# Kernel tuning notes

Measured on AMD Instinct MI355X. Metric: run time of the kernel, lower is better.

The kernel has to match this reference:

```python
import jax, jax.numpy as jnp
import numpy as np

# config constants
B, L, ENC_IN = 8, 512, 7
D_MODEL = 768
EXPAND = 2
D_INNER = D_MODEL * EXPAND          # 1536
DT_RANK = (D_MODEL + 15) // 16      # 48
N_STATE = 16                         # configs.d_ff acts as SSM state size
K_CONV = 4
E_LAYERS = 2
C_OUT = 7
PRED_LEN = 96
EPS = 1e-5


def rmsnorm(x, w):
    return x * jax.lax.rsqrt(jnp.mean(x * x, axis=-1, keepdims=True) + EPS) * w


def silu(x):
    return x * jax.nn.sigmoid(x)


def positional_embedding(l, d):
    pos = np.arange(l, dtype=np.float32)[:, None]
    div = np.exp(np.arange(0, d, 2, dtype=np.float32) * (-np.log(10000.0) / d))
    pe = np.zeros((l, d), dtype=np.float32)
    pe[:, 0::2] = np.sin(pos * div)
    pe[:, 1::2] = np.cos(pos * div)
    return jnp.asarray(pe)


def causal_dwconv(x, w, b):
    # x: [b, d, l], w: [d, 1, k]; torch pads k-1 both sides then slices [:l] == left-pad k-1
    y = jax.lax.conv_general_dilated(
        x, w, window_strides=(1,), padding=[(K_CONV - 1, 0)],
        dimension_numbers=('NCH', 'OIH', 'NCH'), feature_group_count=D_INNER)
    return y + b[None, :, None]


def selective_scan(u, delta, A, Bm, Cm, Dp):
    # u, delta: [b,l,d]; A: [d,n]; Bm, Cm: [b,l,n]; Dp: [d]
    deltaA = jnp.exp(jnp.einsum('bld,dn->bldn', delta, A))          # [b,l,d,n]
    deltaBu = (delta * u)[..., None] * Bm[:, :, None, :]             # [b,l,d,n]

    def step(xc, inp):
        dA, dBu, Ct = inp                                            # [b,d,n],[b,d,n],[b,n]
        xc = dA * xc + dBu
        return xc, jnp.einsum('bdn,bn->bd', xc, Ct)

    b, l, d = u.shape
    x0 = jnp.zeros((b, d, A.shape[1]), u.dtype)
    _, ys = jax.lax.scan(step, x0, (jnp.moveaxis(deltaA, 1, 0),
                                    jnp.moveaxis(deltaBu, 1, 0),
                                    jnp.moveaxis(Cm, 1, 0)))
    y = jnp.moveaxis(ys, 0, 1)                                       # [b,l,d]
    return y + u * Dp


def mamba_block(x, in_w, conv_w, conv_b, xproj_w, dtproj_w, dtproj_b, A_log, Dp, outproj_w):
    xr = x @ in_w.T                                                  # [b,l,2*d_inner]
    xs, res = xr[..., :D_INNER], xr[..., D_INNER:]
    xs = causal_dwconv(jnp.swapaxes(xs, 1, 2), conv_w, conv_b)
    xs = silu(jnp.swapaxes(xs, 1, 2))
    # ssm
    A = -jnp.exp(A_log)
    x_dbl = xs @ xproj_w.T                                           # [b,l,dt_rank+2n]
    delta = x_dbl[..., :DT_RANK]
    Bm = x_dbl[..., DT_RANK:DT_RANK + N_STATE]
    Cm = x_dbl[..., DT_RANK + N_STATE:]
    delta = jax.nn.softplus(delta @ dtproj_w.T + dtproj_b)
    y = selective_scan(xs, delta, A, Bm, Cm, Dp)
    y = y * silu(res)
    return y @ outproj_w.T


def setup_inputs() -> dict:
    key = jax.random.key(0)
    ks = iter(jax.random.split(key, 32))
    s = 0.02
    d = {}
    d['x'] = jax.random.normal(next(ks), (B, L, ENC_IN), jnp.float32)
    d['token_w'] = jax.random.normal(next(ks), (D_MODEL, ENC_IN, 3), jnp.float32) * s
    d['time_w'] = jax.random.normal(next(ks), (D_MODEL, 1), jnp.float32) * s
    d['norm_w'] = jnp.ones((E_LAYERS, D_MODEL), jnp.float32)
    d['in_w'] = jax.random.normal(next(ks), (E_LAYERS, 2 * D_INNER, D_MODEL), jnp.float32) * s
    d['conv_w'] = jax.random.normal(next(ks), (E_LAYERS, D_INNER, 1, K_CONV), jnp.float32) * s
    d['conv_b'] = jnp.zeros((E_LAYERS, D_INNER), jnp.float32)
    d['xproj_w'] = jax.random.normal(next(ks), (E_LAYERS, DT_RANK + 2 * N_STATE, D_INNER), jnp.float32) * s
    d['dtproj_w'] = jax.random.normal(next(ks), (E_LAYERS, D_INNER, DT_RANK), jnp.float32) * s
    d['dtproj_b'] = jnp.zeros((E_LAYERS, D_INNER), jnp.float32)
    A = np.tile(np.arange(1, N_STATE + 1, dtype=np.float32)[None, :], (D_INNER, 1))
    d['A_log'] = jnp.tile(jnp.log(jnp.asarray(A))[None], (E_LAYERS, 1, 1))
    d['Dp'] = jnp.ones((E_LAYERS, D_INNER), jnp.float32)
    d['outproj_w'] = jax.random.normal(next(ks), (E_LAYERS, D_MODEL, D_INNER), jnp.float32) * s
    d['final_norm_w'] = jnp.ones((D_MODEL,), jnp.float32)
    d['out_w'] = jax.random.normal(next(ks), (C_OUT, D_MODEL), jnp.float32) * s
    return d


def reference(x, token_w, time_w, norm_w, in_w, conv_w, conv_b, xproj_w,
              dtproj_w, dtproj_b, A_log, Dp, outproj_w, final_norm_w, out_w):
    # instance normalization (mean/std detached)
    mean_enc = jax.lax.stop_gradient(jnp.mean(x, axis=1, keepdims=True))
    xc = x - mean_enc
    std_enc = jax.lax.stop_gradient(jnp.sqrt(jnp.var(xc, axis=1, keepdims=True) + 1e-5))
    xc = xc / std_enc
    # DataEmbedding: circular conv token emb + sinusoidal pos + timeF linear
    xp = jnp.pad(jnp.swapaxes(xc, 1, 2), ((0, 0), (0, 0), (1, 1)), mode='wrap')
    tok = jax.lax.conv_general_dilated(xp, token_w, (1,), 'VALID',
                                       dimension_numbers=('NCH', 'OIH', 'NCH'))
    tok = jnp.swapaxes(tok, 1, 2)                                    # [b,l,d_model]
    x_mark = (jnp.arange(L, dtype=x.dtype) / L)[None, :, None]       # [1,l,1]
    h = tok + positional_embedding(L, D_MODEL)[None] + x_mark @ time_w.T
    for e in range(E_LAYERS):
        h = mamba_block(rmsnorm(h, norm_w[e]), in_w[e], conv_w[e], conv_b[e],
                        xproj_w[e], dtproj_w[e], dtproj_b[e], A_log[e], Dp[e],
                        outproj_w[e]) + h
    h = rmsnorm(h, final_norm_w)
    out = h @ out_w.T
    out = out * std_enc + mean_enc
    return out[:, -PRED_LEN:, :]
```

## Files before the change

kernel.cpp:

```cpp
#include <hip/hip_runtime.h>
#include <hip/hip_bf16.h>
#include <math.h>

#define BSZ 8
#define LSEQ 512
#define ENC_IN 7
#define D_MODEL 768
#define D_INNER 1536
#define DT_RANK 48
#define N_STATE 16
#define K_CONV 4
#define E_LAYERS 2
#define C_OUT 7
#define PRED_LEN 96
#define EPSV 1e-5f
#define XN 80
#define KSPLIT 4

#define ROWS (BSZ*LSEQ)
#define NC 16
#define CL (LSEQ/NC)
#define NTILE (LSEQ/16)
#define LOG2E 1.44269504088896f

typedef __bf16 bf16x8 __attribute__((ext_vector_type(8)));
typedef float  f32x4  __attribute__((ext_vector_type(4)));

__device__ __forceinline__ float fexp2(float x) {
    float r;
    asm("v_exp_f32 %0, %1" : "=v"(r) : "v"(x));
    return r;
}

__device__ __forceinline__ float block_sum(float v, float* tmp) {
    #pragma unroll
    for (int off = 32; off > 0; off >>= 1) v += __shfl_down(v, off);
    int lane = threadIdx.x & 63, wid = threadIdx.x >> 6;
    __syncthreads();
    if (lane == 0) tmp[wid] = v;
    __syncthreads();
    return tmp[0] + tmp[1] + tmp[2] + tmp[3];
}

__global__ __launch_bounds__(256) void cvt_all(const float* __restrict__ in_w,
                                               const float* __restrict__ outw,
                                               const float* __restrict__ xpw,
                                               const float* __restrict__ dtw,
                                               __hip_bfloat16* __restrict__ inw_bf,
                                               __hip_bfloat16* __restrict__ outw_bf,
                                               __hip_bfloat16* __restrict__ xpw_bf,
                                               __hip_bfloat16* __restrict__ dtw_bf) {
    const int N1 = E_LAYERS*2*D_INNER*D_MODEL;
    const int N2 = E_LAYERS*D_MODEL*D_INNER;
    const int N3 = E_LAYERS*XN*D_INNER;
    const int N4 = E_LAYERS*D_INNER*64;
    int i = blockIdx.x*256 + threadIdx.x;
    if (i < N1) {
        inw_bf[i] = __float2bfloat16(in_w[i]);
    } else if (i < N1+N2) {
        int j = i - N1; outw_bf[j] = __float2bfloat16(outw[j]);
    } else if (i < N1+N2+N3) {
        int j = i - N1 - N2; xpw_bf[j] = __float2bfloat16(xpw[j]);
    } else if (i < N1+N2+N3+N4) {
        int j = i - N1 - N2 - N3;
        int r = j >> 6, c = j & 63;
        dtw_bf[j] = __float2bfloat16(c < DT_RANK ? dtw[r*DT_RANK + c] : 0.f);
    }
}

__global__ __launch_bounds__(256) void stats_kernel(const float* __restrict__ x,
                                                    float* __restrict__ mean,
                                                    float* __restrict__ stdv) {
    int bc = blockIdx.x;
    int b = bc / ENC_IN, c = bc % ENC_IN;
    __shared__ float tmp[4];
    float s = 0.f, sq = 0.f;
    for (int l = threadIdx.x; l < LSEQ; l += 256) {
        float v = x[((size_t)(b*LSEQ + l))*ENC_IN + c];
        s += v; sq += v*v;
    }
    s = block_sum(s, tmp);
    sq = block_sum(sq, tmp);
    if (threadIdx.x == 0) {
        float m = s / LSEQ;
        float var = sq / LSEQ - m*m;
        if (var < 0.f) var = 0.f;
        mean[bc] = m;
        stdv[bc] = sqrtf(var + EPSV);
    }
}

__global__ __launch_bounds__(256) void embed_kernel(const float* __restrict__ x,
                                                    const float* __restrict__ token_w,
                                                    const float* __restrict__ time_w,
                                                    const float* __restrict__ mean,
                                                    const float* __restrict__ stdv,
                                                    float* __restrict__ h) {
    int bl = blockIdx.x;
    int b = bl >> 9, l = bl & 511;
    __shared__ float sxc[ENC_IN*3];
    if (threadIdx.x < ENC_IN*3) {
        int c = threadIdx.x / 3, k = threadIdx.x % 3;
        int lk = (l + k - 1) & 511;
        float v = x[((size_t)(b*LSEQ + lk))*ENC_IN + c];
        sxc[threadIdx.x] = (v - mean[b*ENC_IN + c]) / stdv[b*ENC_IN + c];
    }
    __syncthreads();
    #pragma unroll
    for (int i = 0; i < 3; i++) {
        int d = threadIdx.x + i*256;
        float acc = 0.f;
        const float* w = token_w + (size_t)d*21;
        #pragma unroll
        for (int t = 0; t < 21; t++) acc += sxc[t] * w[t];
        int d2 = d & ~1;
        float div = __expf((float)d2 * (-9.210340371976184f / (float)D_MODEL));
        float ang = (float)l * div;
        float pe = (d & 1) ? cosf(ang) : sinf(ang);
        float tm = ((float)l / (float)LSEQ) * time_w[d];
        h[(size_t)bl*D_MODEL + d] = acc + pe + tm;
    }
}

__global__ __launch_bounds__(256) void rmsnorm_bf16(const float* __restrict__ h,
                                                    const float* __restrict__ w,
                                                    __hip_bfloat16* __restrict__ xn) {
    size_t base = (size_t)blockIdx.x * D_MODEL;
    __shared__ float tmp[4];
    float ss = 0.f;
    for (int k = threadIdx.x; k < D_MODEL; k += 256) { float v = h[base+k]; ss += v*v; }
    ss = block_sum(ss, tmp);
    float inv = rsqrtf(ss / (float)D_MODEL + EPSV);
    for (int k = threadIdx.x; k < D_MODEL; k += 256)
        xn[base+k] = __float2bfloat16(h[base+k]*inv*w[k]);
}

template<int FUSE>
__global__ __launch_bounds__(256) void gemm_mfma(const __hip_bfloat16* __restrict__ A,
                                                 const __hip_bfloat16* __restrict__ Bw,
                                                 float* __restrict__ C,
                                                 int K,
                                                 const float* __restrict__ bias,
                                                 float* __restrict__ C2,
                                                 __hip_bfloat16* __restrict__ Cb) {
    __shared__ __align__(16) __hip_bfloat16 As[128*32];
    __shared__ __align__(16) __hip_bfloat16 Bs[128*32];
    int tid = threadIdx.x, lane = tid & 63, w = tid >> 6;
    int gx = gridDim.x;
    int nwg = gx * gridDim.y;
    int orig = blockIdx.y*gx + blockIdx.x;
    int swz = (orig & 7)*(nwg >> 3) + (orig >> 3);
    int m0 = (swz / gx) * 128, n0 = (swz % gx) * 128;
    int wr = w >> 1, wc = w & 1;
    int kq = lane >> 4, rr = lane & 15;

    f32x4 acc[4][4];
    #pragma unroll
    for (int i = 0; i < 4; i++)
        #pragma unroll
        for (int j = 0; j < 4; j++) acc[i][j] = (f32x4){0.f,0.f,0.f,0.f};

    const char* Ab = (const char*)A;
    const char* Bb = (const char*)Bw;
    char* AsB = (char*)As;
    char* BsB = (char*)Bs;

    int c0 = tid, c1 = tid + 256;
    int r0 = c0 >> 2, q0 = (c0 & 3) ^ ((r0 >> 1) & 3);
    int r1 = c1 >> 2, q1 = (c1 & 3) ^ ((r1 >> 1) & 3);
    int sw = (kq ^ ((rr >> 1) & 3)) * 16;

    for (int k0 = 0; k0 < K; k0 += 32) {
        __builtin_amdgcn_global_load_lds(
            (const __attribute__((address_space(1))) unsigned int*)(Ab + ((size_t)(m0+r0)*K + k0 + q0*8)*2),
            (__attribute__((address_space(3))) unsigned int*)(AsB + c0*16), 16, 0, 0);
        __builtin_amdgcn_global_load_lds(
            (const __attribute__((address_space(1))) unsigned int*)(Ab + ((size_t)(m0+r1)*K + k0 + q1*8)*2),
            (__attribute__((address_space(3))) unsigned int*)(AsB + c1*16), 16, 0, 0);
        __builtin_amdgcn_global_load_lds(
            (const __attribute__((address_space(1))) unsigned int*)(Bb + ((size_t)(n0+r0)*K + k0 + q0*8)*2),
            (__attribute__((address_space(3))) unsigned int*)(BsB + c0*16), 16, 0, 0);
        __builtin_amdgcn_global_load_lds(
            (const __attribute__((address_space(1))) unsigned int*)(Bb + ((size_t)(n0+r1)*K + k0 + q1*8)*2),
            (__attribute__((address_space(3))) unsigned int*)(BsB + c1*16), 16, 0, 0);
        __syncthreads();

        bf16x8 af[4], bfr[4];
        #pragma unroll
        for (int mi = 0; mi < 4; mi++) af[mi]  = *(const bf16x8*)(AsB + (wr*64 + mi*16 + rr)*64 + sw);
        #pragma unroll
        for (int ni = 0; ni < 4; ni++) bfr[ni] = *(const bf16x8*)(BsB + (wc*64 + ni*16 + rr)*64 + sw);
        #pragma unroll
        for (int mi = 0; mi < 4; mi++)
            #pragma unroll
            for (int ni = 0; ni < 4; ni++)
                acc[mi][ni] = __builtin_amdgcn_mfma_f32_16x16x32_bf16(af[mi], bfr[ni], acc[mi][ni], 0, 0, 0);
        __syncthreads();
    }

    #pragma unroll
    for (int mi = 0; mi < 4; mi++) {
        #pragma unroll
        for (int ni = 0; ni < 4; ni++) {
            int row0 = m0 + wr*64 + mi*16;
            int col  = n0 + wc*64 + ni*16 + rr;
            if (FUSE == 1) {
                float4 v4;
                #pragma unroll
                for (int r = 0; r < 4; r++) {
                    float v = acc[mi][ni][r] + bias[col];
                    ((float*)&v4)[r] = fmaxf(v, 0.f) + log1pf(__expf(-fabsf(v)));
                }
                *(float4*)&C[((size_t)(row0 >> 4)*D_INNER + col)*16 + kq*4] = v4;
            } else if (FUSE == 3) {
                if (col >= D_INNER) {
                    float4 v4;
                    #pragma unroll
                    for (int r = 0; r < 4; r++) {
                        float v = acc[mi][ni][r];
                        ((float*)&v4)[r] = v / (1.f + __expf(-v));
                    }
                    *(float4*)&C2[((size_t)(row0 >> 4)*D_INNER + (col - D_INNER))*16 + kq*4] = v4;
                } else {
                    #pragma unroll
                    for (int r = 0; r < 4; r++) {
                        int row = row0 + kq*4 + r;
                        Cb[(size_t)row*D_INNER + col] = __float2bfloat16(acc[mi][ni][r]);
                    }
                }
            }
        }
    }
}

__global__ __launch_bounds__(256) void gemm_outproj(const __hip_bfloat16* __restrict__ A,
                                                    const __hip_bfloat16* __restrict__ Bw,
                                                    float* __restrict__ C) {
    __shared__ __align__(16) __hip_bfloat16 As[128*32];
    __shared__ __align__(16) __hip_bfloat16 Bs[64*32];
    int tid = threadIdx.x, lane = tid & 63, w = tid >> 6;
    int gx = gridDim.x;
    int nwg = gx * gridDim.y;
    int orig = blockIdx.y*gx + blockIdx.x;
    int swz = (orig & 7)*(nwg >> 3) + (orig >> 3);
    int m0 = (swz / gx) * 128, n0 = (swz % gx) * 64;
    int wr = w >> 1, wc = w & 1;
    int kq = lane >> 4, rr = lane & 15;
    const int K = D_INNER;

    f32x4 acc[4][2];
    #pragma unroll
    for (int i = 0; i < 4; i++)
        #pragma unroll
        for (int j = 0; j < 2; j++) acc[i][j] = (f32x4){0.f,0.f,0.f,0.f};

    const char* Ab = (const char*)A;
    const char* Bb = (const char*)Bw;
    char* AsB = (char*)As;
    char* BsB = (char*)Bs;

    int cA0 = tid, cA1 = tid + 256;
    int rA0 = cA0 >> 2, qA0 = (cA0 & 3) ^ ((rA0 >> 1) & 3);
    int rA1 = cA1 >> 2, qA1 = (cA1 & 3) ^ ((rA1 >> 1) & 3);
    int rB = tid >> 2,  qB  = (tid & 3) ^ ((rB >> 1) & 3);
    int sw = (kq ^ ((rr >> 1) & 3)) * 16;

    for (int k0 = 0; k0 < K; k0 += 32) {
        __builtin_amdgcn_global_load_lds(
            (const __attribute__((address_space(1))) unsigned int*)(Ab + ((size_t)(m0+rA0)*K + k0 + qA0*8)*2),
            (__attribute__((address_space(3))) unsigned int*)(AsB + cA0*16), 16, 0, 0);
        __builtin_amdgcn_global_load_lds(
            (const __attribute__((address_space(1))) unsigned int*)(Ab + ((size_t)(m0+rA1)*K + k0 + qA1*8)*2),
            (__attribute__((address_space(3))) unsigned int*)(AsB + cA1*16), 16, 0, 0);
        __builtin_amdgcn_global_load_lds(
            (const __attribute__((address_space(1))) unsigned int*)(Bb + ((size_t)(n0+rB)*K + k0 + qB*8)*2),
            (__attribute__((address_space(3))) unsigned int*)(BsB + tid*16), 16, 0, 0);
        __syncthreads();

        bf16x8 af[4], bfr[2];
        #pragma unroll
        for (int mi = 0; mi < 4; mi++) af[mi]  = *(const bf16x8*)(AsB + (wr*64 + mi*16 + rr)*64 + sw);
        #pragma unroll
        for (int ni = 0; ni < 2; ni++) bfr[ni] = *(const bf16x8*)(BsB + (wc*32 + ni*16 + rr)*64 + sw);
        #pragma unroll
        for (int mi = 0; mi < 4; mi++)
            #pragma unroll
            for (int ni = 0; ni < 2; ni++)
                acc[mi][ni] = __builtin_amdgcn_mfma_f32_16x16x32_bf16(af[mi], bfr[ni], acc[mi][ni], 0, 0, 0);
        __syncthreads();
    }

    #pragma unroll
    for (int mi = 0; mi < 4; mi++) {
        #pragma unroll
        for (int ni = 0; ni < 2; ni++) {
            #pragma unroll
            for (int r = 0; r < 4; r++) {
                int row = m0 + wr*64 + mi*16 + kq*4 + r;
                int col = n0 + wc*32 + ni*16 + rr;
                size_t o = (size_t)row*D_MODEL + col;
                C[o] = acc[mi][ni][r] + C[o];
            }
        }
    }
}

__global__ __launch_bounds__(256) void gemm_xproj(const __hip_bfloat16* __restrict__ A,
                                                  const __hip_bfloat16* __restrict__ W,
                                                  float* __restrict__ P) {
    __shared__ __align__(16) __hip_bfloat16 As[64*64];
    __shared__ __align__(16) __hip_bfloat16 Bs[96*64];
    int tid = threadIdx.x, lane = tid & 63, w = tid >> 6;
    int m0 = blockIdx.x * 64;
    int k0 = blockIdx.y * (D_INNER / KSPLIT);
    int kq = lane >> 4, rr = lane & 15;
    f32x4 acc[5];
    #pragma unroll
    for (int i = 0; i < 5; i++) acc[i] = (f32x4){0.f,0.f,0.f,0.f};
    const char* Ab = (const char*)A;
    const char* Wb = (const char*)W;
    char* AsB = (char*)As;
    char* BsB = (char*)Bs;

    for (int kk = k0; kk < k0 + D_INNER/KSPLIT; kk += 64) {
        #pragma unroll
        for (int cA = 0; cA < 2; cA++) {
            int idx = cA*256 + tid;
            int r = idx >> 3, q = (idx & 7) ^ (r & 7);
            __builtin_amdgcn_global_load_lds(
                (const __attribute__((address_space(1))) unsigned int*)(Ab + ((size_t)(m0+r)*D_INNER + kk + q*8)*2),
                (__attribute__((address_space(3))) unsigned int*)(AsB + idx*16), 16, 0, 0);
        }
        #pragma unroll
        for (int cB = 0; cB < 3; cB++) {
            int idx = cB*256 + tid;
            int r = idx >> 3, q = (idx & 7) ^ (r & 7);
            int rs = r < XN ? r : XN-1;
            __builtin_amdgcn_global_load_lds(
                (const __attribute__((address_space(1))) unsigned int*)(Wb + ((size_t)rs*D_INNER + kk + q*8)*2),
                (__attribute__((address_space(3))) unsigned int*)(BsB + idx*16), 16, 0, 0);
        }
        __syncthreads();
        #pragma unroll
        for (int kh = 0; kh < 2; kh++) {
            bf16x8 a = *(const bf16x8*)(AsB + (w*16 + rr)*128 + (((kh*4 + kq) ^ (rr & 7)))*16);
            #pragma unroll
            for (int ni = 0; ni < 5; ni++) {
                bf16x8 b = *(const bf16x8*)(BsB + (ni*16 + rr)*128 + (((kh*4 + kq) ^ (rr & 7)))*16);
                acc[ni] = __builtin_amdgcn_mfma_f32_16x16x32_bf16(a, b, acc[ni], 0, 0, 0);
            }
        }
        __syncthreads();
    }
    float* Cp = P + (size_t)blockIdx.y * ROWS * XN;
    #pragma unroll
    for (int ni = 0; ni < 5; ni++)
        #pragma unroll
        for (int r = 0; r < 4; r++) {
            int row = m0 + w*16 + kq*4 + r;
            int col = ni*16 + rr;
            Cp[(size_t)row*XN + col] = acc[ni][r];
        }
}

__global__ __launch_bounds__(256) void xproj_reduce(const float* __restrict__ P,
                                                    float* __restrict__ xdbl,
                                                    __hip_bfloat16* __restrict__ xdbl_bf) {
    int idx = blockIdx.x*256 + threadIdx.x;
    int col = idx % 96, row = idx / 96;
    if (row >= ROWS) return;
    const size_t RX = (size_t)ROWS*XN;
    if (col < XN) {
        size_t o = (size_t)row*XN + col;
        float s = P[o] + P[RX + o] + P[2*RX + o] + P[3*RX + o];
        xdbl[o] = s;
        if (col < DT_RANK) xdbl_bf[(size_t)row*64 + col] = __float2bfloat16(s);
    } else {
        xdbl_bf[(size_t)row*64 + col - 32] = __float2bfloat16(0.f);
    }
}

__global__ __launch_bounds__(256) void dwconv_silu(const __hip_bfloat16* __restrict__ xs,
                                                   const float* __restrict__ cw,
                                                   const float* __restrict__ cb,
                                                   __hip_bfloat16* __restrict__ u_bf) {
    int idx = blockIdx.x*256 + threadIdx.x;
    int dg = idx % (D_INNER/8);
    int t  = idx / (D_INNER/8);
    if (t >= ROWS) return;
    int d0 = dg*8;
    int l = t & 511, b = t >> 9;
    bf16x8 rows[K_CONV];
    #pragma unroll
    for (int k = 0; k < K_CONV; k++) {
        int ll = l - (K_CONV-1) + k;
        if (ll >= 0) rows[k] = *(const bf16x8*)(xs + ((size_t)(b*LSEQ + ll))*D_INNER + d0);
        else { bf16x8 z = {}; rows[k] = z; }
    }
    bf16x8 outv;
    #pragma unroll
    for (int j = 0; j < 8; j++) {
        int d = d0 + j;
        const float4 w4 = *(const float4*)(cw + d*K_CONV);
        float acc = cb[d]
                  + (float)rows[0][j]*w4.x + (float)rows[1][j]*w4.y
                  + (float)rows[2][j]*w4.z + (float)rows[3][j]*w4.w;
        float v = acc / (1.f + __expf(-acc));
        outv[j] = (__bf16)v;
    }
    *(bf16x8*)(u_bf + (size_t)t*D_INNER + d0) = outv;
}

__global__ __launch_bounds__(256) void scan_p1(const __hip_bfloat16* __restrict__ u,
                                               const float* __restrict__ delta_blk,
                                               const float* __restrict__ xdbl,
                                               const float* __restrict__ A_log,
                                               float* __restrict__ xfin,
                                               float* __restrict__ sumdlt) {
    int d = blockIdx.x*256 + threadIdx.x;
    int c = blockIdx.y, b = blockIdx.z;
    int l0 = c*CL;
    float A2[N_STATE], xs[N_STATE];
    const float* al = A_log + d*N_STATE;
    #pragma unroll
    for (int n = 0; n < N_STATE; n++) {
        A2[n] = -__expf(al[n]) * LOG2E;
        xs[n] = 0.f;
    }
    const __hip_bfloat16* pu = u + (size_t)(b*LSEQ + l0)*D_INNER + d;
    const float* pB = xdbl + (size_t)(b*LSEQ + l0)*XN + DT_RANK;
    float sd = 0.f;
    #pragma unroll
    for (int tt = 0; tt < 2; tt++) {
        const float* db = delta_blk + ((size_t)(b*NTILE + (l0>>4) + tt)*D_INNER + d)*16;
        float dl[16];
        #pragma unroll
        for (int q = 0; q < 4; q++) {
            f32x4 v = *(const f32x4*)(db + q*4);
            dl[q*4+0]=v[0]; dl[q*4+1]=v[1]; dl[q*4+2]=v[2]; dl[q*4+3]=v[3];
        }
        #pragma unroll
        for (int i = 0; i < 16; i++) {
            float dlt = dl[i];
            float uu = __bfloat162float(*pu); pu += D_INNER;
            float du = dlt*uu;
            sd += dlt;
            #pragma unroll
            for (int n = 0; n < N_STATE; n++)
                xs[n] = fexp2(dlt*A2[n])*xs[n] + du*pB[n];
            pB += XN;
        }
    }
    float* px = xfin + (size_t)((b*NC + c)*N_STATE)*D_INNER + d;
    #pragma unroll
    for (int n = 0; n < N_STATE; n++) px[n*D_INNER] = xs[n];
    sumdlt[(size_t)(b*NC + c)*D_INNER + d] = sd;
}

__global__ __launch_bounds__(256) void scan_p2(float* __restrict__ xfin,
                                               const float* __restrict__ sumdlt,
                                               const float* __restrict__ A_log) {
    int idx = blockIdx.x*256 + threadIdx.x;
    int d = idx % D_INNER;
    int r = idx / D_INNER;
    int n = r & 15;
    int b = r >> 4;
    float A2 = -__expf(A_log[d*N_STATE + n]) * LOG2E;
    float cr = 0.f;
    for (int c = 1; c < NC; c++) {
        size_t jp = (size_t)(b*NC + c - 1);
        float xf = xfin[(jp*N_STATE + n)*D_INNER + d];
        float s  = sumdlt[jp*D_INNER + d];
        cr = fexp2(A2 * s) * cr + xf;
        xfin[(jp*N_STATE + n)*D_INNER + d] = cr;
    }
}

__global__ __launch_bounds__(256) void scan_p3(const __hip_bfloat16* __restrict__ u,
                                               const float* __restrict__ delta_blk,
                                               const float* __restrict__ gres_blk,
                                               const float* __restrict__ xdbl,
                                               const float* __restrict__ A_log,
                                               const float* __restrict__ Dp,
                                               const float* __restrict__ carry,
                                               __hip_bfloat16* __restrict__ ygate) {
    int d = blockIdx.x*256 + threadIdx.x;
    int c = blockIdx.y, b = blockIdx.z;
    int l0 = c*CL;
    float A2[N_STATE], xs[N_STATE];
    const float* al = A_log + d*N_STATE;
    #pragma unroll
    for (int n = 0; n < N_STATE; n++) A2[n] = -__expf(al[n]) * LOG2E;
    if (c == 0) {
        #pragma unroll
        for (int n = 0; n < N_STATE; n++) xs[n] = 0.f;
    } else {
        const float* pc = carry + (size_t)((b*NC + c - 1)*N_STATE)*D_INNER + d;
        #pragma unroll
        for (int n = 0; n < N_STATE; n++) xs[n] = pc[n*D_INNER];
    }
    float Dv = Dp[d];
    const __hip_bfloat16* pu = u + (size_t)(b*LSEQ + l0)*D_INNER + d;
    const float* pB = xdbl + (size_t)(b*LSEQ + l0)*XN + DT_RANK;
    __hip_bfloat16* py = ygate + (size_t)(b*LSEQ + l0)*D_INNER + d;
    #pragma unroll
    for (int tt = 0; tt < 2; tt++) {
        size_t tb = (size_t)(b*NTILE + (l0>>4) + tt)*D_INNER + d;
        const float* db = delta_blk + tb*16;
        const float* gb = gres_blk  + tb*16;
        float dl[16], gr[16];
        #pragma unroll
        for (int q = 0; q < 4; q++) {
            f32x4 v = *(const f32x4*)(db + q*4);
            dl[q*4+0]=v[0]; dl[q*4+1]=v[1]; dl[q*4+2]=v[2]; dl[q*4+3]=v[3];
            f32x4 g = *(const f32x4*)(gb + q*4);
            gr[q*4+0]=g[0]; gr[q*4+1]=g[1]; gr[q*4+2]=g[2]; gr[q*4+3]=g[3];
        }
        #pragma unroll
        for (int i = 0; i < 16; i++) {
            float dlt = dl[i];
            float uu = __bfloat162float(*pu); pu += D_INNER;
            float du = dlt*uu;
            float acc = 0.f;
            #pragma unroll
            for (int n = 0; n < N_STATE; n++) {
                xs[n] = fexp2(dlt*A2[n])*xs[n] + du*pB[n];
                acc += xs[n]*pB[N_STATE + n];
            }
            pB += XN;
            float y = acc + uu*Dv;
            *py = __float2bfloat16(y * gr[i]); py += D_INNER;
        }
    }
}

__global__ __launch_bounds__(256) void final_kernel(const float* __restrict__ h,
                                                    const float* __restrict__ fnw,
                                                    const float* __restrict__ out_w,
                                                    const float* __restrict__ mean,
                                                    const float* __restrict__ stdv,
                                                    float* __restrict__ out) {
    int bid = blockIdx.x;
    int b = bid / PRED_LEN, lo = bid % PRED_LEN;
    int l = LSEQ - PRED_LEN + lo;
    const float* row = h + ((size_t)(b*LSEQ + l))*D_MODEL;
    __shared__ float tmp[4];
    float ss = 0.f;
    for (int k = threadIdx.x; k < D_MODEL; k += 256) { float v = row[k]; ss += v*v; }
    ss = block_sum(ss, tmp);
    float inv = rsqrtf(ss / (float)D_MODEL + EPSV);
    float acc[C_OUT] = {};
    for (int k = threadIdx.x; k < D_MODEL; k += 256) {
        float hn = row[k]*fnw[k];
        #pragma unroll
        for (int c = 0; c < C_OUT; c++) acc[c] += hn*out_w[c*D_MODEL + k];
    }
    #pragma unroll
    for (int c = 0; c < C_OUT; c++) {
        float s = block_sum(acc[c], tmp);
        if (threadIdx.x == 0)
            out[((size_t)(b*PRED_LEN + lo))*C_OUT + c] = s*inv*stdv[b*ENC_IN + c] + mean[b*ENC_IN + c];
    }
}

extern "C" void kernel_launch(void* const* d_in, const int* in_sizes, int n_in,
                              void* d_out, int out_size, void* d_ws, size_t ws_size,
                              hipStream_t stream) {
    const float* x        = (const float*)d_in[0];
    const float* token_w  = (const float*)d_in[1];
    const float* time_w   = (const float*)d_in[2];
    const float* norm_w   = (const float*)d_in[3];
    const float* in_w     = (const float*)d_in[4];
    const float* conv_w   = (const float*)d_in[5];
    const float* conv_b   = (const float*)d_in[6];
    const float* xproj_w  = (const float*)d_in[7];
    const float* dtproj_w = (const float*)d_in[8];
    const float* dtproj_b = (const float*)d_in[9];
    const float* A_log    = (const float*)d_in[10];
    const float* Dp       = (const float*)d_in[11];
    const float* outproj_w= (const float*)d_in[12];
    const float* final_nw = (const float*)d_in[13];
    const float* out_w    = (const float*)d_in[14];
    float* out = (float*)d_out;

    float* ws   = (float*)d_ws;
    float* mean = ws;
    float* stdv = ws + 64;
    float* h    = ws + 128;
    float* gres = h    + (size_t)ROWS*D_MODEL;
    float* delta= gres + (size_t)ROWS*D_INNER;
    float* xdbl = delta+ (size_t)ROWS*D_INNER;
    float* sumd = xdbl + (size_t)ROWS*XN;
    float* xfin = sumd + (size_t)BSZ*NC*D_INNER;
    float* pout = xfin + (size_t)BSZ*NC*D_INNER*N_STATE;
    float* fend = pout + (size_t)KSPLIT*ROWS*XN;
    __hip_bfloat16* xn_bf  = (__hip_bfloat16*)fend;
    __hip_bfloat16* xs_bf  = xn_bf + (size_t)ROWS*D_MODEL;
    __hip_bfloat16* u_bf   = xs_bf + (size_t)ROWS*D_INNER;
    __hip_bfloat16* ygate  = u_bf  + (size_t)ROWS*D_INNER;
    __hip_bfloat16* xdbl_bf= ygate + (size_t)ROWS*D_INNER;
    __hip_bfloat16* inw_bf = xdbl_bf+ (size_t)ROWS*64;
    __hip_bfloat16* outw_bf= inw_bf + (size_t)E_LAYERS*2*D_INNER*D_MODEL;
    __hip_bfloat16* xpw_bf = outw_bf+ (size_t)E_LAYERS*D_MODEL*D_INNER;
    __hip_bfloat16* dtw_bf = xpw_bf + (size_t)E_LAYERS*XN*D_INNER;

    {
        const int NT = E_LAYERS*2*D_INNER*D_MODEL + E_LAYERS*D_MODEL*D_INNER
                     + E_LAYERS*XN*D_INNER + E_LAYERS*D_INNER*64;
        cvt_all<<<(NT+255)/256, 256, 0, stream>>>(in_w, outproj_w, xproj_w, dtproj_w,
                                                  inw_bf, outw_bf, xpw_bf, dtw_bf);
    }

    stats_kernel<<<BSZ*ENC_IN, 256, 0, stream>>>(x, mean, stdv);
    embed_kernel<<<ROWS, 256, 0, stream>>>(x, token_w, time_w, mean, stdv, h);

    for (int e = 0; e < E_LAYERS; e++) {
        rmsnorm_bf16<<<ROWS, 256, 0, stream>>>(h, norm_w + e*D_MODEL, xn_bf);
        gemm_mfma<3><<<dim3(2*D_INNER/128, ROWS/128), 256, 0, stream>>>(
            xn_bf, inw_bf + (size_t)e*2*D_INNER*D_MODEL, nullptr, D_MODEL,
            nullptr, gres, xs_bf);
        dwconv_silu<<<(ROWS*(D_INNER/8) + 255)/256, 256, 0, stream>>>(
            xs_bf, conv_w + (size_t)e*D_INNER*K_CONV, conv_b + e*D_INNER, u_bf);
        gemm_xproj<<<dim3(ROWS/64, KSPLIT), 256, 0, stream>>>(
            u_bf, xpw_bf + (size_t)e*XN*D_INNER, pout);
        xproj_reduce<<<(ROWS*96 + 255)/256, 256, 0, stream>>>(pout, xdbl, xdbl_bf);
        gemm_mfma<1><<<dim3(D_INNER/128, ROWS/128), 256, 0, stream>>>(
            xdbl_bf, dtw_bf + (size_t)e*D_INNER*64, delta, 64,
            dtproj_b + e*D_INNER, nullptr, nullptr);
        const float* Alog_e = A_log + (size_t)e*D_INNER*N_STATE;
        scan_p1<<<dim3(D_INNER/256, NC, BSZ), 256, 0, stream>>>(
            u_bf, delta, xdbl, Alog_e, xfin, sumd);
        scan_p2<<<(BSZ*D_INNER*N_STATE)/256, 256, 0, stream>>>(
            xfin, sumd, Alog_e);
        scan_p3<<<dim3(D_INNER/256, NC, BSZ), 256, 0, stream>>>(
            u_bf, delta, gres, xdbl, Alog_e, Dp + (size_t)e*D_INNER, xfin, ygate);
        gemm_outproj<<<dim3(D_MODEL/64, ROWS/128), 256, 0, stream>>>(
            ygate, outw_bf + (size_t)e*D_MODEL*D_INNER, h);
    }

    final_kernel<<<BSZ*PRED_LEN, 256, 0, stream>>>(h, final_nw, out_w, mean, stdv, out);
}
```

Baseline: 400.2 us.

## Fuse dt projection and softplus into scan kernels, widen in-proj K tile

The dt_proj GEMM and its delta buffer are removed. Each scan thread now holds its 48 dt weights in registers and computes delta = softplus(bias + x_dbl·w) inline in both scan passes, so delta is computed twice but never written to or read from memory. The gate buffer is stored as bf16 instead of fp32, and the in-projection GEMM uses a 64-wide K tile with a new swizzle. The cost is extra FMAs and register pressure in the scan kernels (48 extra registers plus per-step dot products), which may reduce occupancy.

New measurement: 471.7 us. 17.9% more time.

```diff
diff --git a/kernel.cpp b/kernel.cpp
--- a/kernel.cpp
+++ b/kernel.cpp
@@ -31,6 +31,9 @@
     asm("v_exp_f32 %0, %1" : "=v"(r) : "v"(x));
     return r;
 }
+__device__ __forceinline__ float softplusf(float v) {
+    return fmaxf(v, 0.f) + log1pf(__expf(-fabsf(v)));
+}
 
 __device__ __forceinline__ float block_sum(float v, float* tmp) {
     #pragma unroll
@@ -45,15 +48,12 @@
 __global__ __launch_bounds__(256) void cvt_all(const float* __restrict__ in_w,
                                                const float* __restrict__ outw,
                                                const float* __restrict__ xpw,
-                                               const float* __restrict__ dtw,
                                                __hip_bfloat16* __restrict__ inw_bf,
                                                __hip_bfloat16* __restrict__ outw_bf,
-                                               __hip_bfloat16* __restrict__ xpw_bf,
-                                               __hip_bfloat16* __restrict__ dtw_bf) {
+                                               __hip_bfloat16* __restrict__ xpw_bf) {
     const int N1 = E_LAYERS*2*D_INNER*D_MODEL;
     const int N2 = E_LAYERS*D_MODEL*D_INNER;
     const int N3 = E_LAYERS*XN*D_INNER;
-    const int N4 = E_LAYERS*D_INNER*64;
     int i = blockIdx.x*256 + threadIdx.x;
     if (i < N1) {
         inw_bf[i] = __float2bfloat16(in_w[i]);
@@ -61,10 +61,6 @@
         int j = i - N1; outw_bf[j] = __float2bfloat16(outw[j]);
     } else if (i < N1+N2+N3) {
         int j = i - N1 - N2; xpw_bf[j] = __float2bfloat16(xpw[j]);
-    } else if (i < N1+N2+N3+N4) {
-        int j = i - N1 - N2 - N3;
-        int r = j >> 6, c = j & 63;
-        dtw_bf[j] = __float2bfloat16(c < DT_RANK ? dtw[r*DT_RANK + c] : 0.f);
     }
 }
 
@@ -135,16 +131,13 @@
         xn[base+k] = __float2bfloat16(h[base+k]*inv*w[k]);
 }
 
-template<int FUSE>
-__global__ __launch_bounds__(256) void gemm_mfma(const __hip_bfloat16* __restrict__ A,
-                                                 const __hip_bfloat16* __restrict__ Bw,
-                                                 float* __restrict__ C,
-                                                 int K,
-                                                 const float* __restrict__ bias,
-                                                 float* __restrict__ C2,
-                                                 __hip_bfloat16* __restrict__ Cb) {
-    __shared__ __align__(16) __hip_bfloat16 As[128*32];
-    __shared__ __align__(16) __hip_bfloat16 Bs[128*32];
+__global__ __launch_bounds__(256) void gemm_inproj(const __hip_bfloat16* __restrict__ A,
+                                                   const __hip_bfloat16* __restrict__ Bw,
+                                                   __hip_bfloat16* __restrict__ Cxs,
+                                                   __hip_bfloat16* __restrict__ Cg) {
+    __shared__ __align__(16) __hip_bfloat16 As[128*64];
+    __shared__ __align__(16) __hip_bfloat16 Bs[128*64];
+    const int K = D_MODEL;
     int tid = threadIdx.x, lane = tid & 63, w = tid >> 6;
     int gx = gridDim.x;
     int nwg = gx * gridDim.y;
@@ -165,36 +158,35 @@
     char* AsB = (char*)As;
     char* BsB = (char*)Bs;
 
-    int c0 = tid, c1 = tid + 256;
-    int r0 = c0 >> 2, q0 = (c0 & 3) ^ ((r0 >> 1) & 3);
-    int r1 = c1 >> 2, q1 = (c1 & 3) ^ ((r1 >> 1) & 3);
-    int sw = (kq ^ ((rr >> 1) & 3)) * 16;
-
-    for (int k0 = 0; k0 < K; k0 += 32) {
-        __builtin_amdgcn_global_load_lds(
-            (const __attribute__((address_space(1))) unsigned int*)(Ab + ((size_t)(m0+r0)*K + k0 + q0*8)*2),
-            (__attribute__((address_space(3))) unsigned int*)(AsB + c0*16), 16, 0, 0);
-        __builtin_amdgcn_global_load_lds(
-            (const __attribute__((address_space(1))) unsigned int*)(Ab + ((size_t)(m0+r1)*K + k0 + q1*8)*2),
-            (__attribute__((address_space(3))) unsigned int*)(AsB + c1*16), 16, 0, 0);
-        __builtin_amdgcn_global_load_lds(
-            (const __attribute__((address_space(1))) unsigned int*)(Bb + ((size_t)(n0+r0)*K + k0 + q0*8)*2),
-            (__attribute__((address_space(3))) unsigned int*)(BsB + c0*16), 16, 0, 0);
-        __builtin_amdgcn_global_load_lds(
-            (const __attribute__((address_space(1))) unsigned int*)(Bb + ((size_t)(n0+r1)*K + k0 + q1*8)*2),
-            (__attribute__((address_space(3))) unsigned int*)(BsB + c1*16), 16, 0, 0);
+    for (int k0 = 0; k0 < K; k0 += 64) {
+        #pragma unroll
+        for (int c = 0; c < 4; c++) {
+            int idx = c*256 + tid;
+            int r = idx >> 3, q = idx & 7;
+            int qs = q ^ (r & 7);
+            __builtin_amdgcn_global_load_lds(
+                (const __attribute__((address_space(1))) unsigned int*)(Ab + ((size_t)(m0+r)*K + k0 + qs*8)*2),
+                (__attribute__((address_space(3))) unsigned int*)(AsB + idx*16), 16, 0, 0);
+            __builtin_amdgcn_global_load_lds(
+                (const __attribute__((address_space(1))) unsigned int*)(Bb + ((size_t)(n0+r)*K + k0 + qs*8)*2),
+                (__attribute__((address_space(3))) unsigned int*)(BsB + idx*16), 16, 0, 0);
+        }
         __syncthreads();
 
-        bf16x8 af[4], bfr[4];
-        #pragma unroll
-        for (int mi = 0; mi < 4; mi++) af[mi]  = *(const bf16x8*)(AsB + (wr*64 + mi*16 + rr)*64 + sw);
-        #pragma unroll
-        for (int ni = 0; ni < 4; ni++) bfr[ni] = *(const bf16x8*)(BsB + (wc*64 + ni*16 + rr)*64 + sw);
-        #pragma unroll
-        for (int mi = 0; mi < 4; mi++)
-            #pragma unroll
-            for (int ni = 0; ni < 4; ni++)
-                acc[mi][ni] = __builtin_amdgcn_mfma_f32_16x16x32_bf16(af[mi], bfr[ni], acc[mi][ni], 0, 0, 0);
+        #pragma unroll
+        for (int kh = 0; kh < 2; kh++) {
+            int ch = ((kh*4 + kq) ^ (rr & 7)) * 16;
+            bf16x8 af[4], bfr[4];
+            #pragma unroll
+            for (int mi = 0; mi < 4; mi++) af[mi]  = *(const bf16x8*)(AsB + (wr*64 + mi*16 + rr)*128 + ch);
+            #pragma unroll
+            for (int ni = 0; ni < 4; ni++) bfr[ni] = *(const bf16x8*)(BsB + (wc*64 + ni*16 + rr)*128 + ch);
+            #pragma unroll
+            for (int mi = 0; mi < 4; mi++)
+                #pragma unroll
+                for (int ni = 0; ni < 4; ni++)
+                    acc[mi][ni] = __builtin_amdgcn_mfma_f32_16x16x32_bf16(af[mi], bfr[ni], acc[mi][ni], 0, 0, 0);
+        }
         __syncthreads();
     }
 
@@ -204,29 +196,20 @@
         for (int ni = 0; ni < 4; ni++) {
             int row0 = m0 + wr*64 + mi*16;
             int col  = n0 + wc*64 + ni*16 + rr;
-            if (FUSE == 1) {
-                float4 v4;
+            if (col >= D_INNER) {
+                __hip_bfloat16 g4[4];
                 #pragma unroll
                 for (int r = 0; r < 4; r++) {
-                    float v = acc[mi][ni][r] + bias[col];
-                    ((float*)&v4)[r] = fmaxf(v, 0.f) + log1pf(__expf(-fabsf(v)));
+                    float v = acc[mi][ni][r];
+                    g4[r] = __float2bfloat16(v / (1.f + __expf(-v)));
                 }
-                *(float4*)&C[((size_t)(row0 >> 4)*D_INNER + col)*16 + kq*4] = v4;
-            } else if (FUSE == 3) {
-                if (col >= D_INNER) {
-                    float4 v4;
-                    #pragma unroll
-                    for (int r = 0; r < 4; r++) {
-                        float v = acc[mi][ni][r];
-                        ((float*)&v4)[r] = v / (1.f + __expf(-v));
-                    }
-                    *(float4*)&C2[((size_t)(row0 >> 4)*D_INNER + (col - D_INNER))*16 + kq*4] = v4;
-                } else {
-                    #pragma unroll
-                    for (int r = 0; r < 4; r++) {
-                        int row = row0 + kq*4 + r;
-                        Cb[(size_t)row*D_INNER + col] = __float2bfloat16(acc[mi][ni][r]);
-                    }
+                int cd = col - D_INNER;
+                *(uint2*)&Cg[((size_t)(row0 >> 4)*D_INNER + cd)*16 + kq*4] = *(uint2*)g4;
+            } else {
+                #pragma unroll
+                for (int r = 0; r < 4; r++) {
+                    int row = row0 + kq*4 + r;
+                    Cxs[(size_t)row*D_INNER + col] = __float2bfloat16(acc[mi][ni][r]);
                 }
             }
         }
@@ -364,20 +347,11 @@
 }
 
 __global__ __launch_bounds__(256) void xproj_reduce(const float* __restrict__ P,
-                                                    float* __restrict__ xdbl,
-                                                    __hip_bfloat16* __restrict__ xdbl_bf) {
+                                                    float* __restrict__ xdbl) {
     int idx = blockIdx.x*256 + threadIdx.x;
-    int col = idx % 96, row = idx / 96;
-    if (row >= ROWS) return;
+    if (idx >= ROWS*XN) return;
     const size_t RX = (size_t)ROWS*XN;
-    if (col < XN) {
-        size_t o = (size_t)row*XN + col;
-        float s = P[o] + P[RX + o] + P[2*RX + o] + P[3*RX + o];
-        xdbl[o] = s;
-        if (col < DT_RANK) xdbl_bf[(size_t)row*64 + col] = __float2bfloat16(s);
-    } else {
-        xdbl_bf[(size_t)row*64 + col - 32] = __float2bfloat16(0.f);
-    }
+    xdbl[idx] = P[idx] + P[RX + idx] + P[2*RX + idx] + P[3*RX + idx];
 }
 
 __global__ __launch_bounds__(256) void dwconv_silu(const __hip_bfloat16* __restrict__ xs,
@@ -412,44 +386,41 @@
 }
 
 __global__ __launch_bounds__(256) void scan_p1(const __hip_bfloat16* __restrict__ u,
-                                               const float* __restrict__ delta_blk,
                                                const float* __restrict__ xdbl,
+                                               const float* __restrict__ dtw,
+                                               const float* __restrict__ dtb,
                                                const float* __restrict__ A_log,
                                                float* __restrict__ xfin,
                                                float* __restrict__ sumdlt) {
     int d = blockIdx.x*256 + threadIdx.x;
     int c = blockIdx.y, b = blockIdx.z;
     int l0 = c*CL;
-    float A2[N_STATE], xs[N_STATE];
+    float A2[N_STATE], xs[N_STATE], wd[DT_RANK];
     const float* al = A_log + d*N_STATE;
     #pragma unroll
     for (int n = 0; n < N_STATE; n++) {
         A2[n] = -__expf(al[n]) * LOG2E;
         xs[n] = 0.f;
     }
+    const float* pw = dtw + (size_t)d*DT_RANK;
+    #pragma unroll
+    for (int k = 0; k < DT_RANK; k++) wd[k] = pw[k];
+    float bias = dtb[d];
     const __hip_bfloat16* pu = u + (size_t)(b*LSEQ + l0)*D_INNER + d;
-    const float* pB = xdbl + (size_t)(b*LSEQ + l0)*XN + DT_RANK;
+    const float* pX = xdbl + (size_t)(b*LSEQ + l0)*XN;
     float sd = 0.f;
-    #pragma unroll
-    for (int tt = 0; tt < 2; tt++) {
-        const float* db = delta_blk + ((size_t)(b*NTILE + (l0>>4) + tt)*D_INNER + d)*16;
-        float dl[16];
-        #pragma unroll
-        for (int q = 0; q < 4; q++) {
-            f32x4 v = *(const f32x4*)(db + q*4);
-            dl[q*4+0]=v[0]; dl[q*4+1]=v[1]; dl[q*4+2]=v[2]; dl[q*4+3]=v[3];
-        }
-        #pragma unroll
-        for (int i = 0; i < 16; i++) {
-            float dlt = dl[i];
-            float uu = __bfloat162float(*pu); pu += D_INNER;
-            float du = dlt*uu;
-            sd += dlt;
-            #pragma unroll
-            for (int n = 0; n < N_STATE; n++)
-                xs[n] = fexp2(dlt*A2[n])*xs[n] + du*pB[n];
-            pB += XN;
-        }
+    for (int i = 0; i < CL; i++) {
+        float v = bias;
+        #pragma unroll
+        for (int k = 0; k < DT_RANK; k++) v += pX[k]*wd[k];
+        float dlt = softplusf(v);
+        float uu = __bfloat162float(*pu); pu += D_INNER;
+        float du = dlt*uu;
+        sd += dlt;
+        #pragma unroll
+        for (int n = 0; n < N_STATE; n++)
+            xs[n] = fexp2(dlt*A2[n])*xs[n] + du*pX[DT_RANK + n];
+        pX += XN;
     }
     float* px = xfin + (size_t)((b*NC + c)*N_STATE)*D_INNER + d;
     #pragma unroll
@@ -477,9 +448,10 @@
 }
 
 __global__ __launch_bounds__(256) void scan_p3(const __hip_bfloat16* __restrict__ u,
-                                               const float* __restrict__ delta_blk,
-                                               const float* __restrict__ gres_blk,
                                                const float* __restrict__ xdbl,
+                                               const float* __restrict__ dtw,
+                                               const float* __restrict__ dtb,
+                                               const __hip_bfloat16* __restrict__ gres,
                                                const float* __restrict__ A_log,
                                                const float* __restrict__ Dp,
                                                const float* __restrict__ carry,
@@ -487,10 +459,14 @@
     int d = blockIdx.x*256 + threadIdx.x;
     int c = blockIdx.y, b = blockIdx.z;
     int l0 = c*CL;
-    float A2[N_STATE], xs[N_STATE];
+    float A2[N_STATE], xs[N_STATE], wd[DT_RANK];
     const float* al = A_log + d*N_STATE;
     #pragma unroll
     for (int n = 0; n < N_STATE; n++) A2[n] = -__expf(al[n]) * LOG2E;
+    const float* pw = dtw + (size_t)d*DT_RANK;
+    #pragma unroll
+    for (int k = 0; k < DT_RANK; k++) wd[k] = pw[k];
+    float bias = dtb[d];
     if (c == 0) {
         #pragma unroll
         for (int n = 0; n < N_STATE; n++) xs[n] = 0.f;
@@ -501,33 +477,32 @@
     }
     float Dv = Dp[d];
     const __hip_bfloat16* pu = u + (size_t)(b*LSEQ + l0)*D_INNER + d;
-    const float* pB = xdbl + (size_t)(b*LSEQ + l0)*XN + DT_RANK;
+    const float* pX = xdbl + (size_t)(b*LSEQ + l0)*XN;
     __hip_bfloat16* py = ygate + (size_t)(b*LSEQ + l0)*D_INNER + d;
     #pragma unroll
     for (int tt = 0; tt < 2; tt++) {
         size_t tb = (size_t)(b*NTILE + (l0>>4) + tt)*D_INNER + d;
-        const float* db = delta_blk + tb*16;
-        const float* gb = gres_blk  + tb*16;
-        float dl[16], gr[16];
-        #pragma unroll
-        for (int q = 0; q < 4; q++) {
-            f32x4 v = *(const f32x4*)(db + q*4);
-            dl[q*4+0]=v[0]; dl[q*4+1]=v[1]; dl[q*4+2]=v[2]; dl[q*4+3]=v[3];
-            f32x4 g = *(const f32x4*)(gb + q*4);
-            gr[q*4+0]=g[0]; gr[q*4+1]=g[1]; gr[q*4+2]=g[2]; gr[q*4+3]=g[3];
-        }
+        const __hip_bfloat16* gb = gres + tb*16;
+        bf16x8 g0 = *(const bf16x8*)gb;
+        bf16x8 g1 = *(const bf16x8*)(gb + 8);
+        float gr[16];
+        #pragma unroll
+        for (int j = 0; j < 8; j++) { gr[j] = (float)g0[j]; gr[8+j] = (float)g1[j]; }
         #pragma unroll
         for (int i = 0; i < 16; i++) {
-            float dlt = dl[i];
+            float v = bias;
+            #pragma unroll
+            for (int k = 0; k < DT_RANK; k++) v += pX[k]*wd[k];
+            float dlt = softplusf(v);
             float uu = __bfloat162float(*pu); pu += D_INNER;
             float du = dlt*uu;
             float acc = 0.f;
             #pragma unroll
             for (int n = 0; n < N_STATE; n++) {
-                xs[n] = fexp2(dlt*A2[n])*xs[n] + du*pB[n];
-                acc += xs[n]*pB[N_STATE + n];
+                xs[n] = fexp2(dlt*A2[n])*xs[n] + du*pX[DT_RANK + n];
+                acc += xs[n]*pX[DT_RANK + N_STATE + n];
             }
-            pB += XN;
+            pX += XN;
             float y = acc + uu*Dv;
             *py = __float2bfloat16(y * gr[i]); py += D_INNER;
         }
@@ -587,9 +562,7 @@
     float* mean = ws;
     float* stdv = ws + 64;
     float* h    = ws + 128;
-    float* gres = h    + (size_t)ROWS*D_MODEL;
-    float* delta= gres + (size_t)ROWS*D_INNER;
-    float* xdbl = delta+ (size_t)ROWS*D_INNER;
+    float* xdbl = h    + (size_t)ROWS*D_MODEL;
     float* sumd = xdbl + (size_t)ROWS*XN;
     float* xfin = sumd + (size_t)BSZ*NC*D_INNER;
     float* pout = xfin + (size_t)BSZ*NC*D_INNER*N_STATE;
@@ -597,18 +570,17 @@
     __hip_bfloat16* xn_bf  = (__hip_bfloat16*)fend;
     __hip_bfloat16* xs_bf  = xn_bf + (size_t)ROWS*D_MODEL;
     __hip_bfloat16* u_bf   = xs_bf + (size_t)ROWS*D_INNER;
-    __hip_bfloat16* ygate  = u_bf  + (size_t)ROWS*D_INNER;
-    __hip_bfloat16* xdbl_bf= ygate + (size_t)ROWS*D_INNER;
-    __hip_bfloat16* inw_bf = xdbl_bf+ (size_t)ROWS*64;
+    __hip_bfloat16* gres   = u_bf  + (size_t)ROWS*D_INNER;
+    __hip_bfloat16* ygate  = gres  + (size_t)ROWS*D_INNER;
+    __hip_bfloat16* inw_bf = ygate + (size_t)ROWS*D_INNER;
     __hip_bfloat16* outw_bf= inw_bf + (size_t)E_LAYERS*2*D_INNER*D_MODEL;
     __hip_bfloat16* xpw_bf = outw_bf+ (size_t)E_LAYERS*D_MODEL*D_INNER;
-    __hip_bfloat16* dtw_bf = xpw_bf + (size_t)E_LAYERS*XN*D_INNER;
 
     {
         const int NT = E_LAYERS*2*D_INNER*D_MODEL + E_LAYERS*D_MODEL*D_INNER
-                     + E_LAYERS*XN*D_INNER + E_LAYERS*D_INNER*64;
-        cvt_all<<<(NT+255)/256, 256, 0, stream>>>(in_w, outproj_w, xproj_w, dtproj_w,
-                                                  inw_bf, outw_bf, xpw_bf, dtw_bf);
+                     + E_LAYERS*XN*D_INNER;
+        cvt_all<<<(NT+255)/256, 256, 0, stream>>>(in_w, outproj_w, xproj_w,
+                                                  inw_bf, outw_bf, xpw_bf);
     }
 
     stats_kernel<<<BSZ*ENC_IN, 256, 0, stream>>>(x, mean, stdv);
@@ -616,24 +588,22 @@
 
     for (int e = 0; e < E_LAYERS; e++) {
         rmsnorm_bf16<<<ROWS, 256, 0, stream>>>(h, norm_w + e*D_MODEL, xn_bf);
-        gemm_mfma<3><<<dim3(2*D_INNER/128, ROWS/128), 256, 0, stream>>>(
-            xn_bf, inw_bf + (size_t)e*2*D_INNER*D_MODEL, nullptr, D_MODEL,
-            nullptr, gres, xs_bf);
+        gemm_inproj<<<dim3(2*D_INNER/128, ROWS/128), 256, 0, stream>>>(
+            xn_bf, inw_bf + (size_t)e*2*D_INNER*D_MODEL, xs_bf, gres);
         dwconv_silu<<<(ROWS*(D_INNER/8) + 255)/256, 256, 0, stream>>>(
             xs_bf, conv_w + (size_t)e*D_INNER*K_CONV, conv_b + e*D_INNER, u_bf);
         gemm_xproj<<<dim3(ROWS/64, KSPLIT), 256, 0, stream>>>(
             u_bf, xpw_bf + (size_t)e*XN*D_INNER, pout);
-        xproj_reduce<<<(ROWS*96 + 255)/256, 256, 0, stream>>>(pout, xdbl, xdbl_bf);
-        gemm_mfma<1><<<dim3(D_INNER/128, ROWS/128), 256, 0, stream>>>(
-            xdbl_bf, dtw_bf + (size_t)e*D_INNER*64, delta, 64,
-            dtproj_b + e*D_INNER, nullptr, nullptr);
+        xproj_reduce<<<(ROWS*XN + 255)/256, 256, 0, stream>>>(pout, xdbl);
         const float* Alog_e = A_log + (size_t)e*D_INNER*N_STATE;
+        const float* dtw_e  = dtproj_w + (size_t)e*D_INNER*DT_RANK;
+        const float* dtb_e  = dtproj_b + (size_t)e*D_INNER;
         scan_p1<<<dim3(D_INNER/256, NC, BSZ), 256, 0, stream>>>(
-            u_bf, delta, xdbl, Alog_e, xfin, sumd);
+            u_bf, xdbl, dtw_e, dtb_e, Alog_e, xfin, sumd);
         scan_p2<<<(BSZ*D_INNER*N_STATE)/256, 256, 0, stream>>>(
             xfin, sumd, Alog_e);
         scan_p3<<<dim3(D_INNER/256, NC, BSZ), 256, 0, stream>>>(
-            u_bf, delta, gres, xdbl, Alog_e, Dp + (size_t)e*D_INNER, xfin, ygate);
+            u_bf, xdbl, dtw_e, dtb_e, gres, Alog_e, Dp + (size_t)e*D_INNER, xfin, ygate);
         gemm_outproj<<<dim3(D_MODEL/64, ROWS/128), 256, 0, stream>>>(
             ygate, outw_bf + (size_t)e*D_MODEL*D_INNER, h);
     }
```
